# Optimization experiments

Hardware: AMD Instinct MI355X
Metric: run time of the kernel (lower is better)

Reference implementation:

```python
import jax, jax.numpy as jnp
import numpy as np

B, S, DIM = 4, 4096, 1024
H, HD = 16, 64  # n_heads, head_dim = dim // n_heads
UMV = 20.0      # unified_max_value (init kwarg)


def setup_inputs() -> dict:
    key = jax.random.key(0)
    kx, kw = jax.random.split(key)
    x = jax.random.normal(kx, (B, S, DIM), dtype=jnp.float32)
    # qkv_proj: Linear(dim, 3*dim). Small weight scale + positive bias keeps
    # attention scores inside the keep-window [0, 2*UMV] so denominators are safe.
    W_qkv = jax.random.normal(kw, (DIM, 3 * DIM), dtype=jnp.float32) * 0.02
    b_qkv = jnp.full((3 * DIM,), 0.5, dtype=jnp.float32)
    return {"x": x, "W_qkv": W_qkv, "b_qkv": b_qkv}


def reference(x, W_qkv, b_qkv):
    Bb, Ss, _ = x.shape
    qkv = x @ W_qkv + b_qkv                      # [B,S,3*dim]
    qkv = qkv.reshape(Bb, Ss, H, 3 * HD)          # [B,S,H,3*hd]
    Q, K, V = jnp.split(qkv, 3, axis=-1)          # each [B,S,H,hd]
    # matmul(Q, K.transpose(-2,-1)) on [B,S,H,hd]: contract head_dim -> [B,S,H,H]
    s = jnp.einsum('bshd,bsgd->bshg', Q, K) - UMV
    e = jnp.exp(s)
    mask = (s > UMV) | (s < -UMV)                 # keep only s in [-UMV, UMV]
    e = jnp.where(mask, 0.0, e)
    denom = jnp.sum(e, axis=-1, keepdims=True)
    p = e / denom                                  # [B,S,H,H]
    out = jnp.einsum('bshg,bsgd->bshd', p, V)      # [B,S,H,hd]
    return out
```

## Files before the change

kernel.cpp:

```cpp
#include <hip/hip_runtime.h>

typedef _Float16 v8h __attribute__((ext_vector_type(8)));
typedef _Float16 v4h __attribute__((ext_vector_type(4)));
typedef _Float16 v2h __attribute__((ext_vector_type(2)));
typedef float v4f __attribute__((ext_vector_type(4)));

__device__ __forceinline__ void gl16(const void* g, void* l) {
    __builtin_amdgcn_global_load_lds(
        (const __attribute__((address_space(1))) unsigned int*)g,
        (__attribute__((address_space(3))) unsigned int*)l, 16, 0, 0);
}

__device__ __forceinline__ void wave_lds_fence() {
    asm volatile("s_waitcnt lgkmcnt(0)" ::: "memory");
}

__global__ __launch_bounds__(256) void k_cvt(const float* __restrict__ x,
                                             _Float16* __restrict__ x16,
                                             const float* __restrict__ W,
                                             _Float16* __restrict__ Wt) {
    if (blockIdx.x < 8192) {
        int i = (blockIdx.x * 256 + threadIdx.x) * 8;
        float4 a = *(const float4*)(x + i);
        float4 b = *(const float4*)(x + i + 4);
        v8h h;
        h[0] = (_Float16)a.x; h[1] = (_Float16)a.y; h[2] = (_Float16)a.z; h[3] = (_Float16)a.w;
        h[4] = (_Float16)b.x; h[5] = (_Float16)b.y; h[6] = (_Float16)b.z; h[7] = (_Float16)b.w;
        *(v8h*)(x16 + i) = h;
    } else {
        __shared__ float T[64][68];
        int bid = blockIdx.x - 8192;
        int k0 = (bid & 15) * 64;
        int n0 = (bid >> 4) * 64;
        int t = threadIdx.x;
        int tr = t >> 4;
        int tc = t & 15;
#pragma unroll
        for (int rr = 0; rr < 4; rr++) {
            int kk = rr * 16 + tr;
            float4 v = *(const float4*)(W + (size_t)(k0 + kk) * 3072 + n0 + tc * 4);
            T[kk][tc * 4 + 0] = v.x; T[kk][tc * 4 + 1] = v.y;
            T[kk][tc * 4 + 2] = v.z; T[kk][tc * 4 + 3] = v.w;
        }
        __syncthreads();
#pragma unroll
        for (int ww = 0; ww < 4; ww++) {
            int nn = ww * 16 + tr;
            v4h h;
#pragma unroll
            for (int i = 0; i < 4; i++) h[i] = (_Float16)T[tc * 4 + i][nn];
            *(v4h*)(Wt + (size_t)(n0 + nn) * 1024 + k0 + tc * 4) = h;
        }
    }
}


#define MFMA16(q, A0K0, A0K1, A1K0, A1K1)                                                   \
    _Pragma("unroll")                                                                       \
    for (int ni = 0; ni < 4; ni++) {                                                        \
        acc[2*(q)][ni]   = __builtin_amdgcn_mfma_f32_16x16x32_f16(A0K0, bf[ni][0], acc[2*(q)][ni], 0, 0, 0);   \
        acc[2*(q)][ni]   = __builtin_amdgcn_mfma_f32_16x16x32_f16(A0K1, bf[ni][1], acc[2*(q)][ni], 0, 0, 0);   \
        acc[2*(q)+1][ni] = __builtin_amdgcn_mfma_f32_16x16x32_f16(A1K0, bf[ni][0], acc[2*(q)+1][ni], 0, 0, 0); \
        acc[2*(q)+1][ni] = __builtin_amdgcn_mfma_f32_16x16x32_f16(A1K1, bf[ni][1], acc[2*(q)+1][ni], 0, 0, 0); \
    }

#define PHASE(XB, q, PRE, WAIT)                                                             \
    {                                                                                       \
        v8h a0k0 = *(const v8h*)&XB[aoff + (2*(q)) * 1024];                                 \
        v8h a0k1 = *(const v8h*)&XB[(aoff ^ 32) + (2*(q)) * 1024];                          \
        v8h a1k0 = *(const v8h*)&XB[aoff + (2*(q)+1) * 1024];                               \
        v8h a1k1 = *(const v8h*)&XB[(aoff ^ 32) + (2*(q)+1) * 1024];                        \
        PRE                                                                                 \
        __builtin_amdgcn_s_barrier();                                                       \
        __builtin_amdgcn_s_setprio(1);                                                      \
        MFMA16(q, a0k0, a0k1, a1k0, a1k1)                                                   \
        __builtin_amdgcn_s_setprio(0);                                                      \
        WAIT                                                                                \
        __builtin_amdgcn_s_barrier();                                                       \
    }

#define LOADB(XB)                                                                           \
    _Pragma("unroll")                                                                       \
    for (int ni = 0; ni < 4; ni++) {                                                        \
        bf[ni][0] = *(const v8h*)&XB[boff + ni * 1024];                                     \
        bf[ni][1] = *(const v8h*)&XB[(boff ^ 32) + ni * 1024];                              \
    }

#define STAGE_A(t, h, j) gl16(aS + (size_t)((h) * 128 + (j) * 8) * 1024 + (t) * 64,         \
                              &As[(t) & 1][((h) * 128 + ldsRow + (j) * 8) * 64])
#define STAGE_B(t, h, j) gl16(bS + (size_t)((h) * 128 + (j) * 8) * 1024 + (t) * 64,         \
                              &Bs[(t) & 1][((h) * 128 + ldsRow + (j) * 8) * 64])

__global__ __launch_bounds__(512, 2) void k_gemm(const _Float16* __restrict__ A,
                                                 const _Float16* __restrict__ Bt,
                                                 const float* __restrict__ bias,
                                                 _Float16* __restrict__ C) {
    __shared__ __align__(16) _Float16 As[2][256 * 64];
    __shared__ __align__(16) _Float16 Bs[2][256 * 64];

    int wg = blockIdx.x;
    wg = (wg & 7) * 96 + (wg >> 3);
    int bm = wg / 12, bn = wg % 12;
    int m0 = bm * 256, n0 = bn * 256;

    int tid = threadIdx.x;
    int w = tid >> 6;
    int lane = tid & 63;
    int l15 = lane & 15, quad = lane >> 4;
    int wm = (w >> 2) * 128;
    int wn = (w & 3) * 64;

    int rl = lane >> 3;
    int ksw = ((lane & 7) ^ rl) * 8;
    const _Float16* aS = A  + (size_t)(m0 + w * 16 + rl) * 1024 + ksw;
    const _Float16* bS = Bt + (size_t)(n0 + w * 16 + rl) * 1024 + ksw;
    int ldsRow = w * 16;

    int swz = (quad ^ (l15 & 7)) * 8;
    int aoff = (wm + l15) * 64 + swz;
    int boff = (wn + l15) * 64 + swz;

    v4f acc[8][4] = {};
    v8h bf[4][2];

    STAGE_A(0, 0, 0); STAGE_A(0, 0, 1); STAGE_A(0, 1, 0); STAGE_A(0, 1, 1);
    STAGE_B(0, 0, 0); STAGE_B(0, 0, 1); STAGE_B(0, 1, 0); STAGE_B(0, 1, 1);
    STAGE_A(1, 0, 0); STAGE_A(1, 0, 1); STAGE_A(1, 1, 0); STAGE_A(1, 1, 1);
    STAGE_B(1, 0, 0); STAGE_B(1, 0, 1); STAGE_B(1, 1, 0); STAGE_B(1, 1, 1);
    asm volatile("s_waitcnt vmcnt(8)" ::: "memory");
    __builtin_amdgcn_s_barrier();

    for (int it = 0; it < 8; ++it) {
        int t = it * 2;
        LOADB(Bs[0])
        PHASE(As[0], 0,
              if (it >= 1) { STAGE_A(t + 1, 0, 0); STAGE_A(t + 1, 0, 1); },
              )
        PHASE(As[0], 1,
              if (it >= 1) { STAGE_A(t + 1, 1, 0); STAGE_A(t + 1, 1, 1); }
              if (it <= 6) { STAGE_B(t + 2, 0, 0); STAGE_B(t + 2, 0, 1); },
              )
        PHASE(As[0], 2,
              if (it <= 6) { STAGE_B(t + 2, 1, 0); STAGE_B(t + 2, 1, 1); },
              )
        PHASE(As[0], 3,
              ,
              if (it == 7) { asm volatile("s_waitcnt vmcnt(0)" ::: "memory"); }
              else         { asm volatile("s_waitcnt vmcnt(4)" ::: "memory"); })
        LOADB(Bs[1])
        PHASE(As[1], 0,
              if (it <= 6) { STAGE_A(t + 2, 0, 0); STAGE_A(t + 2, 0, 1); },
              )
        PHASE(As[1], 1,
              if (it <= 6) { STAGE_A(t + 2, 1, 0); STAGE_A(t + 2, 1, 1); },
              )
        PHASE(As[1], 2,
              if (it <= 6) { STAGE_B(t + 3, 0, 0); STAGE_B(t + 3, 0, 1); },
              )
        PHASE(As[1], 3,
              if (it <= 6) { STAGE_B(t + 3, 1, 0); STAGE_B(t + 3, 1, 1); },
              if (it <= 6) { asm volatile("s_waitcnt vmcnt(4)" ::: "memory"); })
    }

#pragma unroll
    for (int ni = 0; ni < 4; ni++) {
        int n = n0 + wn + ni * 16 + l15;
        float bv = bias[n];
#pragma unroll
        for (int mi = 0; mi < 8; mi++) {
            int mbase = m0 + wm + mi * 16 + quad * 4;
#pragma unroll
            for (int r = 0; r < 4; r++)
                C[(size_t)(mbase + r) * 3072 + n] = (_Float16)(acc[mi][ni][r] + bv);
        }
    }
}

__global__ __launch_bounds__(256) void k_attn(const _Float16* __restrict__ qkv,
                                              float* __restrict__ out) {
    __shared__ __align__(16) _Float16 Pb[4][16 * 24];
    int tid = threadIdx.x;
    int w = tid >> 6, lane = tid & 63;
    int pos = blockIdx.x * 4 + w;
    _Float16* P = Pb[w];
    const _Float16* src = qkv + (size_t)pos * 3072;
    int l15 = lane & 15, quad = lane >> 4;

    const _Float16* hrow = src + l15 * 192;
    v8h a0 = *(const v8h*)(hrow + quad * 8);
    v8h a1 = *(const v8h*)(hrow + 32 + quad * 8);
    v8h b0 = *(const v8h*)(hrow + 64 + quad * 8);
    v8h b1 = *(const v8h*)(hrow + 96 + quad * 8);
    int dl = lane & 15;
    v4h vseg[16];
#pragma unroll
    for (int g = 0; g < 16; g++)
        vseg[g] = *(const v4h*)(src + g * 192 + 128 + dl * 4);

    {
        v4f s = {};
        s = __builtin_amdgcn_mfma_f32_16x16x32_f16(a0, b0, s, 0, 0, 0);
        s = __builtin_amdgcn_mfma_f32_16x16x32_f16(a1, b1, s, 0, 0, 0);
        float e4[4];
#pragma unroll
        for (int r = 0; r < 4; r++) {
            float sv = s[r] - 20.0f;
            e4[r] = (sv > 20.0f || sv < -20.0f) ? 0.0f : __expf(sv);
        }
#pragma unroll
        for (int r = 0; r < 4; r++) {
            float t = e4[r];
            t += __shfl_xor(t, 1, 64);
            t += __shfl_xor(t, 2, 64);
            t += __shfl_xor(t, 4, 64);
            t += __shfl_xor(t, 8, 64);
            P[(quad * 4 + r) * 24 + l15] = (_Float16)(e4[r] / t);
        }
    }
    wave_lds_fence();

    {
        v8h p0[4], p1[4];
#pragma unroll
        for (int t = 0; t < 4; t++) {
            const _Float16* Pr = P + (4 * t + quad) * 24;
            p0[t] = *(const v8h*)Pr;
            p1[t] = *(const v8h*)(Pr + 8);
        }
        v2h o[4][2] = {};
#pragma unroll
        for (int g = 0; g < 16; g++) {
            v2h va; va[0] = vseg[g][0]; va[1] = vseg[g][1];
            v2h vb; vb[0] = vseg[g][2]; vb[1] = vseg[g][3];
#pragma unroll
            for (int t = 0; t < 4; t++) {
                _Float16 ph = (g < 8) ? p0[t][g] : p1[t][g - 8];
                v2h p2; p2[0] = ph; p2[1] = ph;
                o[t][0] = p2 * va + o[t][0];
                o[t][1] = p2 * vb + o[t][1];
            }
        }
        float* dst = out + (size_t)pos * 1024;
#pragma unroll
        for (int t = 0; t < 4; t++) {
            float4 v;
            v.x = (float)o[t][0][0];
            v.y = (float)o[t][0][1];
            v.z = (float)o[t][1][0];
            v.w = (float)o[t][1][1];
            *(float4*)(dst + t * 256 + lane * 4) = v;
        }
    }
}

extern "C" void kernel_launch(void* const* d_in, const int* in_sizes, int n_in,
                              void* d_out, int out_size, void* d_ws, size_t ws_size,
                              hipStream_t stream) {
    (void)in_sizes; (void)n_in; (void)out_size; (void)ws_size;
    const float* x  = (const float*)d_in[0];
    const float* Wq = (const float*)d_in[1];
    const float* bq = (const float*)d_in[2];
    float* out = (float*)d_out;

    char* ob = (char*)d_out;
    _Float16* x16   = (_Float16*)ob;
    _Float16* wt16  = (_Float16*)(ob + (48u << 20));
    _Float16* qkv16 = (_Float16*)d_ws;

    k_cvt<<<8960, 256, 0, stream>>>(x, x16, Wq, wt16);
    k_gemm<<<768, 512, 0, stream>>>(x16, wt16, bq, qkv16);
    k_attn<<<4096, 256, 0, stream>>>(qkv16, out);
}
```

Measured before the change: 264.0 us.

## Switch QKV GEMM to 32x32x16 MFMA with inline-asm double-buffered LDS fragment reads

Rewrites the main loop of the QKV projection GEMM so it uses 32x32x16 MFMA tiles instead of 16x16x32. Fragments are read with inline ds_read_b128 at precomputed swizzled LDS addresses, using two register sets in a ping-pong pattern so the next k-slice is read while the current one is in MFMA. Global-to-LDS staging is regrouped into whole-tile batches, with a full vmcnt(0) wait before each buffer switch. The larger MFMA shape cuts the number of instructions and LDS reads per FLOP. In exchange it raises register pressure, and the stricter vmcnt waits may expose more global-load latency.

```diff
diff --git a/kernel.cpp b/kernel.cpp
--- a/kernel.cpp
+++ b/kernel.cpp
@@ -4,6 +4,7 @@
 typedef _Float16 v4h __attribute__((ext_vector_type(4)));
 typedef _Float16 v2h __attribute__((ext_vector_type(2)));
 typedef float v4f __attribute__((ext_vector_type(4)));
+typedef float f32x16 __attribute__((ext_vector_type(16)));
 
 __device__ __forceinline__ void gl16(const void* g, void* l) {
     __builtin_amdgcn_global_load_lds(
@@ -13,6 +14,10 @@
 
 __device__ __forceinline__ void wave_lds_fence() {
     asm volatile("s_waitcnt lgkmcnt(0)" ::: "memory");
+}
+
+__device__ __forceinline__ unsigned lds_addr(const void* p) {
+    return (unsigned)(size_t)(const __attribute__((address_space(3))) char*)p;
 }
 
 __global__ __launch_bounds__(256) void k_cvt(const float* __restrict__ x,
@@ -55,41 +60,33 @@
 }
 
 
-#define MFMA16(q, A0K0, A0K1, A1K0, A1K1)                                                   \
-    _Pragma("unroll")                                                                       \
-    for (int ni = 0; ni < 4; ni++) {                                                        \
-        acc[2*(q)][ni]   = __builtin_amdgcn_mfma_f32_16x16x32_f16(A0K0, bf[ni][0], acc[2*(q)][ni], 0, 0, 0);   \
-        acc[2*(q)][ni]   = __builtin_amdgcn_mfma_f32_16x16x32_f16(A0K1, bf[ni][1], acc[2*(q)][ni], 0, 0, 0);   \
-        acc[2*(q)+1][ni] = __builtin_amdgcn_mfma_f32_16x16x32_f16(A1K0, bf[ni][0], acc[2*(q)+1][ni], 0, 0, 0); \
-        acc[2*(q)+1][ni] = __builtin_amdgcn_mfma_f32_16x16x32_f16(A1K1, bf[ni][1], acc[2*(q)+1][ni], 0, 0, 0); \
-    }
-
-#define PHASE(XB, q, PRE, WAIT)                                                             \
-    {                                                                                       \
-        v8h a0k0 = *(const v8h*)&XB[aoff + (2*(q)) * 1024];                                 \
-        v8h a0k1 = *(const v8h*)&XB[(aoff ^ 32) + (2*(q)) * 1024];                          \
-        v8h a1k0 = *(const v8h*)&XB[aoff + (2*(q)+1) * 1024];                               \
-        v8h a1k1 = *(const v8h*)&XB[(aoff ^ 32) + (2*(q)+1) * 1024];                        \
-        PRE                                                                                 \
-        __builtin_amdgcn_s_barrier();                                                       \
-        __builtin_amdgcn_s_setprio(1);                                                      \
-        MFMA16(q, a0k0, a0k1, a1k0, a1k1)                                                   \
-        __builtin_amdgcn_s_setprio(0);                                                      \
-        WAIT                                                                                \
-        __builtin_amdgcn_s_barrier();                                                       \
-    }
-
-#define LOADB(XB)                                                                           \
-    _Pragma("unroll")                                                                       \
-    for (int ni = 0; ni < 4; ni++) {                                                        \
-        bf[ni][0] = *(const v8h*)&XB[boff + ni * 1024];                                     \
-        bf[ni][1] = *(const v8h*)&XB[(boff ^ 32) + ni * 1024];                              \
+#define MFMA32(a, b, c) __builtin_amdgcn_mfma_f32_32x32x16_f16(a, b, c, 0, 0, 0)
+#define DSR(d, a, IMM) asm volatile("ds_read_b128 %0, %1 offset:%2" : "=v"(d) : "v"(a), "n"(IMM))
+#define LGKM(N) asm volatile("s_waitcnt lgkmcnt(" #N ")" ::: "memory")
+#define VMCNT(N) asm volatile("s_waitcnt vmcnt(" #N ")" ::: "memory")
+#define SB0() __builtin_amdgcn_sched_barrier(0)
+#define BAR() __builtin_amdgcn_s_barrier()
+#define PRIO1() __builtin_amdgcn_s_setprio(1)
+#define PRIO0() __builtin_amdgcn_s_setprio(0)
+
+#define RD6(AF, BF, VAK, VBK, IMM)                                      \
+    DSR(AF[0], VAK, (IMM));        DSR(AF[1], VAK, (IMM) + 4096);       \
+    DSR(AF[2], VAK, (IMM) + 8192); DSR(AF[3], VAK, (IMM) + 12288);      \
+    DSR(BF[0], VBK, (IMM));        DSR(BF[1], VBK, (IMM) + 4096);
+
+#define MF8(AF, BF)                                                     \
+    _Pragma("unroll")                                                   \
+    for (int mi = 0; mi < 4; mi++) {                                    \
+        acc[mi][0] = MFMA32(AF[mi], BF[0], acc[mi][0]);                 \
+        acc[mi][1] = MFMA32(AF[mi], BF[1], acc[mi][1]);                 \
     }
 
 #define STAGE_A(t, h, j) gl16(aS + (size_t)((h) * 128 + (j) * 8) * 1024 + (t) * 64,         \
                               &As[(t) & 1][((h) * 128 + ldsRow + (j) * 8) * 64])
 #define STAGE_B(t, h, j) gl16(bS + (size_t)((h) * 128 + (j) * 8) * 1024 + (t) * 64,         \
                               &Bs[(t) & 1][((h) * 128 + ldsRow + (j) * 8) * 64])
+#define STAGE_A4(t) STAGE_A(t, 0, 0); STAGE_A(t, 0, 1); STAGE_A(t, 1, 0); STAGE_A(t, 1, 1)
+#define STAGE_B4(t) STAGE_B(t, 0, 0); STAGE_B(t, 0, 1); STAGE_B(t, 1, 0); STAGE_B(t, 1, 1)
 
 __global__ __launch_bounds__(512, 2) void k_gemm(const _Float16* __restrict__ A,
                                                  const _Float16* __restrict__ Bt,
@@ -106,7 +103,6 @@
     int tid = threadIdx.x;
     int w = tid >> 6;
     int lane = tid & 63;
-    int l15 = lane & 15, quad = lane >> 4;
     int wm = (w >> 2) * 128;
     int wn = (w & 3) * 64;
 
@@ -116,62 +112,92 @@
     const _Float16* bS = Bt + (size_t)(n0 + w * 16 + rl) * 1024 + ksw;
     int ldsRow = w * 16;
 
-    int swz = (quad ^ (l15 & 7)) * 8;
-    int aoff = (wm + l15) * 64 + swz;
-    int boff = (wn + l15) * 64 + swz;
-
-    v4f acc[8][4] = {};
-    v8h bf[4][2];
-
-    STAGE_A(0, 0, 0); STAGE_A(0, 0, 1); STAGE_A(0, 1, 0); STAGE_A(0, 1, 1);
-    STAGE_B(0, 0, 0); STAGE_B(0, 0, 1); STAGE_B(0, 1, 0); STAGE_B(0, 1, 1);
-    STAGE_A(1, 0, 0); STAGE_A(1, 0, 1); STAGE_A(1, 1, 0); STAGE_A(1, 1, 1);
-    STAGE_B(1, 0, 0); STAGE_B(1, 0, 1); STAGE_B(1, 1, 0); STAGE_B(1, 1, 1);
-    asm volatile("s_waitcnt vmcnt(8)" ::: "memory");
-    __builtin_amdgcn_s_barrier();
+    int row = lane & 31;
+    int h = lane >> 5;
+    int x = row & 7;
+    unsigned aB = lds_addr(&As[0][0]) + (unsigned)((wm + row) * 128);
+    unsigned bB = lds_addr(&Bs[0][0]) + (unsigned)((wn + row) * 128);
+    unsigned vAk0 = aB + (unsigned)(((0 + h) ^ x) * 16);
+    unsigned vAk1 = aB + (unsigned)(((2 + h) ^ x) * 16);
+    unsigned vAk2 = aB + (unsigned)(((4 + h) ^ x) * 16);
+    unsigned vAk3 = aB + (unsigned)(((6 + h) ^ x) * 16);
+    unsigned vBk0 = bB + (unsigned)(((0 + h) ^ x) * 16);
+    unsigned vBk1 = bB + (unsigned)(((2 + h) ^ x) * 16);
+    unsigned vBk2 = bB + (unsigned)(((4 + h) ^ x) * 16);
+    unsigned vBk3 = bB + (unsigned)(((6 + h) ^ x) * 16);
+
+    f32x16 acc[4][2] = {};
+    v8h a0f[4], b0f[2];
+    v8h a1f[4], b1f[2];
+
+    STAGE_A4(0); STAGE_B4(0);
+    STAGE_A4(1); STAGE_B4(1);
+    VMCNT(8);
+    BAR();
+    RD6(a0f, b0f, vAk0, vBk0, 0)
 
     for (int it = 0; it < 8; ++it) {
         int t = it * 2;
-        LOADB(Bs[0])
-        PHASE(As[0], 0,
-              if (it >= 1) { STAGE_A(t + 1, 0, 0); STAGE_A(t + 1, 0, 1); },
-              )
-        PHASE(As[0], 1,
-              if (it >= 1) { STAGE_A(t + 1, 1, 0); STAGE_A(t + 1, 1, 1); }
-              if (it <= 6) { STAGE_B(t + 2, 0, 0); STAGE_B(t + 2, 0, 1); },
-              )
-        PHASE(As[0], 2,
-              if (it <= 6) { STAGE_B(t + 2, 1, 0); STAGE_B(t + 2, 1, 1); },
-              )
-        PHASE(As[0], 3,
-              ,
-              if (it == 7) { asm volatile("s_waitcnt vmcnt(0)" ::: "memory"); }
-              else         { asm volatile("s_waitcnt vmcnt(4)" ::: "memory"); })
-        LOADB(Bs[1])
-        PHASE(As[1], 0,
-              if (it <= 6) { STAGE_A(t + 2, 0, 0); STAGE_A(t + 2, 0, 1); },
-              )
-        PHASE(As[1], 1,
-              if (it <= 6) { STAGE_A(t + 2, 1, 0); STAGE_A(t + 2, 1, 1); },
-              )
-        PHASE(As[1], 2,
-              if (it <= 6) { STAGE_B(t + 3, 0, 0); STAGE_B(t + 3, 0, 1); },
-              )
-        PHASE(As[1], 3,
-              if (it <= 6) { STAGE_B(t + 3, 1, 0); STAGE_B(t + 3, 1, 1); },
-              if (it <= 6) { asm volatile("s_waitcnt vmcnt(4)" ::: "memory"); })
-    }
-
-#pragma unroll
-    for (int ni = 0; ni < 4; ni++) {
-        int n = n0 + wn + ni * 16 + l15;
+        RD6(a1f, b1f, vAk1, vBk1, 0)
+        if (it >= 1) { STAGE_A4(t + 1); STAGE_B4(t + 1); }
+        LGKM(6); SB0(); PRIO1();
+        MF8(a0f, b0f)
+        PRIO0(); BAR();
+        RD6(a0f, b0f, vAk2, vBk2, 0)
+        LGKM(6); SB0(); PRIO1();
+        MF8(a1f, b1f)
+        PRIO0(); BAR();
+        RD6(a1f, b1f, vAk3, vBk3, 0)
+        LGKM(6); SB0(); PRIO1();
+        MF8(a0f, b0f)
+        PRIO0();
+        VMCNT(0);
+        BAR();
+        RD6(a0f, b0f, vAk0, vBk0, 32768)
+        LGKM(6); SB0(); PRIO1();
+        MF8(a1f, b1f)
+        PRIO0(); BAR();
+        RD6(a1f, b1f, vAk1, vBk1, 32768)
+        if (it <= 6) { STAGE_A4(t + 2); }
+        LGKM(6); SB0(); PRIO1();
+        MF8(a0f, b0f)
+        PRIO0(); BAR();
+        RD6(a0f, b0f, vAk2, vBk2, 32768)
+        if (it <= 6) { STAGE_B4(t + 2); }
+        LGKM(6); SB0(); PRIO1();
+        MF8(a1f, b1f)
+        PRIO0(); BAR();
+        RD6(a1f, b1f, vAk3, vBk3, 32768)
+        LGKM(6); SB0(); PRIO1();
+        MF8(a0f, b0f)
+        PRIO0();
+        VMCNT(0);
+        BAR();
+        if (it <= 6) {
+            RD6(a0f, b0f, vAk0, vBk0, 0)
+            LGKM(6);
+        } else {
+            LGKM(0);
+        }
+        SB0(); PRIO1();
+        MF8(a1f, b1f)
+        PRIO0(); BAR();
+    }
+
+    int cl = lane & 31;
+    int rq = (lane >> 5) * 4;
+#pragma unroll
+    for (int nj = 0; nj < 2; nj++) {
+        int n = n0 + wn + nj * 32 + cl;
         float bv = bias[n];
 #pragma unroll
-        for (int mi = 0; mi < 8; mi++) {
-            int mbase = m0 + wm + mi * 16 + quad * 4;
-#pragma unroll
-            for (int r = 0; r < 4; r++)
-                C[(size_t)(mbase + r) * 3072 + n] = (_Float16)(acc[mi][ni][r] + bv);
+        for (int mi = 0; mi < 4; mi++) {
+            int mb = m0 + wm + mi * 32 + rq;
+#pragma unroll
+            for (int r = 0; r < 16; r++) {
+                int m = mb + (r & 3) + 8 * (r >> 2);
+                C[(size_t)m * 3072 + n] = (_Float16)(acc[mi][nj][r] + bv);
+            }
         }
     }
 }
```

New measurement: 258.2 us. -2.2%, faster.
